# Optimization experiments

Measured on AMD Instinct MI355X. Metric: run time of the kernel, lower is better.

Reference implementation:

```python
import jax, jax.numpy as jnp
import numpy as np

NUM_EMBEDDINGS = 512
EMBEDDING_DIM = 64
COMMITMENT_COST = 0.25


def setup_inputs() -> dict:
    key = jax.random.key(0)
    k1, k2 = jax.random.split(key)
    inputs = jax.random.normal(k1, (256, 2048, EMBEDDING_DIM), dtype=jnp.float32)
    # Glorot uniform for (num_embeddings, embedding_dim)
    limit = np.sqrt(6.0 / (NUM_EMBEDDINGS + EMBEDDING_DIM)).astype(np.float32)
    embeddings = jax.random.uniform(k2, (NUM_EMBEDDINGS, EMBEDDING_DIM),
                                    dtype=jnp.float32, minval=-limit, maxval=limit)
    return {"inputs": inputs, "embeddings": embeddings}


def reference(inputs, embeddings):
    D = embeddings.shape[1]
    flat = inputs.reshape(-1, D)  # [N, D]
    # squared L2 distances via the expanded form (matches the TF code exactly)
    distances = (jnp.sum(flat * flat, axis=1, keepdims=True)
                 + jnp.sum(embeddings * embeddings, axis=1)
                 - 2.0 * flat @ embeddings.T)  # [N, K]
    encoding_indices = jnp.argmin(distances, axis=1)  # [N]
    # direct gather (same math as one-hot matmul, avoids the dense [N,K] matmul)
    quantized = embeddings[encoding_indices].reshape(inputs.shape)
    commitment_loss = COMMITMENT_COST * jnp.mean(
        (jax.lax.stop_gradient(quantized) - inputs) ** 2)
    embedding_loss = jnp.mean((jax.lax.stop_gradient(inputs) - quantized) ** 2)
    # straight-through estimator
    quantized_st = inputs + jax.lax.stop_gradient(quantized - inputs)
    return quantized_st, commitment_loss, embedding_loss
```

## Files before the change

### kernel.cpp

```cpp
#include <hip/hip_runtime.h>
#include <cfloat>

typedef _Float16 f16;
typedef f16 f16x8 __attribute__((ext_vector_type(8)));
typedef float f32x4 __attribute__((ext_vector_type(4)));

#define NTOK (256 * 2048)
#define DDIM 64
#define K 512
#define TPB 256
#define GRID_MAIN 4096
#define GRID_RES  2048
#define THR 1.0e-3f

#define WS_NEEDED 681984

__global__ void vq_pack_kernel(const float* __restrict__ emb, f16* __restrict__ pack) {
    const int chunk = blockIdx.x;
    const int l = threadIdx.x;
    const int split = chunk & 1;
    const int ds = (chunk >> 1) & 1;
    const int ct = chunk >> 2;
    const int code = ct * 16 + (l & 15);
    const int dbase = ds * 32 + (l >> 4) * 8;
    const float* src = emb + (size_t)code * DDIM + dbase;
    f16x8 v;
#pragma unroll
    for (int j = 0; j < 8; ++j) {
        float t = -2.0f * src[j];
        f16 h = (f16)t;
        if (split == 0) v[j] = h;
        else            v[j] = (f16)((t - (float)h) * 2048.0f);
    }
    *(f16x8*)(pack + (size_t)chunk * 512 + (size_t)l * 8) = v;
}

__global__ void vq_senorm_kernel(const float* __restrict__ emb,
                                 float* __restrict__ se) {
    int k = threadIdx.x;
    const float4* e4 = (const float4*)(emb + (size_t)k * DDIM);
    float t[DDIM];
#pragma unroll
    for (int q = 0; q < DDIM / 4; ++q) {
        float4 v = e4[q];
        t[4 * q + 0] = __fmul_rn(v.x, v.x);
        t[4 * q + 1] = __fmul_rn(v.y, v.y);
        t[4 * q + 2] = __fmul_rn(v.z, v.z);
        t[4 * q + 3] = __fmul_rn(v.w, v.w);
    }
#pragma unroll
    for (int s = 1; s < DDIM; s <<= 1)
#pragma unroll
        for (int j = 0; j < DDIM; j += 2 * s) t[j] = __fadd_rn(t[j], t[j + s]);
    se[k] = t[0];
}

#define STAGE_SUPER(buf, s)                                                              \
    do {                                                                                 \
        const char* _g = (const char*)pack + (size_t)(s) * 8192 + (size_t)w * 1024 +     \
                         (size_t)l * 16;                                                 \
        char* _d = (char*)(&Bbuf[(buf)][0]) + (size_t)w * 1024 + (size_t)l * 16;         \
        __builtin_amdgcn_global_load_lds(                                                \
            (const __attribute__((address_space(1))) unsigned int*)_g,                   \
            (__attribute__((address_space(3))) unsigned int*)_d, 16, 0, 0);              \
        __builtin_amdgcn_global_load_lds(                                                \
            (const __attribute__((address_space(1))) unsigned int*)(_g + 4096),          \
            (__attribute__((address_space(3))) unsigned int*)(_d + 4096), 16, 0, 0);     \
    } while (0)

__global__ __launch_bounds__(TPB, 4) void vq_main_kernel(
        const float* __restrict__ xg, const float* __restrict__ emb,
        const f16* __restrict__ pack, const float* __restrict__ se,
        float* __restrict__ out, float* __restrict__ bsum,
        unsigned char* __restrict__ flags) {
    __shared__ f16x8 Bbuf[2][512];
    __shared__ int   kw_lds[4][2][16];
    __shared__ float dw_lds[4][2][16];
    __shared__ float wave_part[4];

    const int tid = threadIdx.x;
    const int w  = tid >> 6;
    const int l  = tid & 63;
    const int lg = l >> 4;
    const int lc = l & 15;
    const size_t base = ((size_t)blockIdx.x * 4 + w) * 32;

    f16x8 Ah[2][2], Al[2][2];
    float sx[2];
#pragma unroll
    for (int i = 0; i < 2; ++i) {
        const float* xp = xg + (base + i * 16 + lc) * DDIM + lg * 8;
        float acc = 0.f;
#pragma unroll
        for (int ds = 0; ds < 2; ++ds) {
            float4 u0 = *(const float4*)(xp + ds * 32);
            float4 u1 = *(const float4*)(xp + ds * 32 + 4);
            float v[8] = {u0.x, u0.y, u0.z, u0.w, u1.x, u1.y, u1.z, u1.w};
            f16x8 h, lo;
#pragma unroll
            for (int j = 0; j < 8; ++j) {
                f16 hh = (f16)v[j];
                h[j]  = hh;
                lo[j] = (f16)((v[j] - (float)hh) * 2048.0f);
                acc = __fmaf_rn(v[j], v[j], acc);
            }
            Ah[i][ds] = h; Al[i][ds] = lo;
        }
        sx[i] = acc;
    }
#pragma unroll
    for (int i = 0; i < 2; ++i) {
        sx[i] += __shfl_xor(sx[i], 16, 64);
        sx[i] += __shfl_xor(sx[i], 32, 64);
    }

    float dmin[2][4], dsec[2][4];
    int   kmin[2][4];
#pragma unroll
    for (int i = 0; i < 2; ++i)
#pragma unroll
        for (int r = 0; r < 4; ++r) { dmin[i][r] = FLT_MAX; dsec[i][r] = FLT_MAX; kmin[i][r] = 0; }

    const int rot = blockIdx.x & 15;
    const float* sebase = se + lc;
    float cs0 = sebase[rot * 32], cs1 = sebase[rot * 32 + 16];
    STAGE_SUPER(0, rot);

    for (int sp = 0; sp < 16; ++sp) {
        const int cur = sp & 1;
        const int s  = (sp + rot) & 15;

        asm volatile("s_waitcnt vmcnt(0)" ::: "memory");
        __builtin_amdgcn_s_barrier();

        float ns0 = 0.f, ns1 = 0.f;
        if (sp < 15) {
            STAGE_SUPER(cur ^ 1, (sp + 1 + rot) & 15);
            const int sn = ((sp + 1 + rot) & 15) * 32;
            ns0 = sebase[sn]; ns1 = sebase[sn + 16];
        }

#pragma unroll
        for (int cl = 0; cl < 2; ++cl) {
            const int ct = s * 2 + cl;
            const int code = ct * 16 + lc;
            const float sek = cl ? cs1 : cs0;
            f16x8 Bh0 = Bbuf[cur][cl * 256 +   0 + l];
            f16x8 Bl0 = Bbuf[cur][cl * 256 +  64 + l];
            f16x8 Bh1 = Bbuf[cur][cl * 256 + 128 + l];
            f16x8 Bl1 = Bbuf[cur][cl * 256 + 192 + l];
#pragma unroll
            for (int i = 0; i < 2; ++i) {
                f32x4 am = {sek, sek, sek, sek};
                f32x4 ac = {0.f, 0.f, 0.f, 0.f};
                am = __builtin_amdgcn_mfma_f32_16x16x32_f16(Ah[i][0], Bh0, am, 0, 0, 0);
                am = __builtin_amdgcn_mfma_f32_16x16x32_f16(Ah[i][1], Bh1, am, 0, 0, 0);
                ac = __builtin_amdgcn_mfma_f32_16x16x32_f16(Al[i][0], Bh0, ac, 0, 0, 0);
                ac = __builtin_amdgcn_mfma_f32_16x16x32_f16(Al[i][1], Bh1, ac, 0, 0, 0);
                ac = __builtin_amdgcn_mfma_f32_16x16x32_f16(Ah[i][0], Bl0, ac, 0, 0, 0);
                ac = __builtin_amdgcn_mfma_f32_16x16x32_f16(Ah[i][1], Bl1, ac, 0, 0, 0);
#pragma unroll
                for (int r = 0; r < 4; ++r) {
                    float v = __fmaf_rn(ac[r], 4.8828125e-4f, am[r]);
                    bool lt = v < dmin[i][r];
                    dsec[i][r] = __builtin_amdgcn_fmed3f(v, dmin[i][r], dsec[i][r]);
                    dmin[i][r] = fminf(v, dmin[i][r]);
                    kmin[i][r] = lt ? code : kmin[i][r];
                }
            }
        }
        cs0 = ns0; cs1 = ns1;
    }

#pragma unroll
    for (int i = 0; i < 2; ++i)
#pragma unroll
        for (int r = 0; r < 4; ++r) {
#pragma unroll
            for (int off = 1; off <= 8; off <<= 1) {
                float dvm = __shfl_xor(dmin[i][r], off, 64);
                int   kvm = __shfl_xor(kmin[i][r], off, 64);
                float dvs = __shfl_xor(dsec[i][r], off, 64);
                bool take = dvm < dmin[i][r];
                float lose = take ? dmin[i][r] : dvm;
                if (take) { dmin[i][r] = dvm; kmin[i][r] = kvm; }
                dsec[i][r] = fminf(fminf(dsec[i][r], dvs), lose);
            }
        }

    if (lc == 0) {
#pragma unroll
        for (int i = 0; i < 2; ++i)
#pragma unroll
            for (int r = 0; r < 4; ++r) {
                int fl = (dsec[i][r] <= dmin[i][r] + THR) ? 1 : 0;
                kw_lds[w][i][lg * 4 + r] = kmin[i][r] | (fl << 31);
                dw_lds[w][i][lg * 4 + r] = dmin[i][r];
                flags[base + i * 16 + lg * 4 + r] = (unsigned char)fl;
            }
    }
    __syncthreads();

#pragma unroll
    for (int m = 0; m < 8; ++m) {
        const int row = m * 4 + (l >> 4);
        const int kwv = kw_lds[w][row >> 4][row & 15] & 0x7fffffff;
        f32x4 vsrc = ((const f32x4*)(emb + (size_t)kwv * DDIM))[lc];
        __builtin_nontemporal_store(vsrc, (f32x4*)(out + (base + row) * DDIM) + lc);
    }

    float lp = 0.f;
    if (l < 16) {
        int k0 = kw_lds[w][0][l], k1 = kw_lds[w][1][l];
        float t0 = (k0 < 0) ? 0.f : __fadd_rn(sx[0], dw_lds[w][0][l]);
        float t1 = (k1 < 0) ? 0.f : __fadd_rn(sx[1], dw_lds[w][1][l]);
        lp = __fadd_rn(t0, t1);
    }
#pragma unroll
    for (int off = 32; off >= 1; off >>= 1) lp += __shfl_down(lp, off, 64);
    if (l == 0) wave_part[w] = lp;
    __syncthreads();
    if (tid == 0) {
        bsum[blockIdx.x] = __fadd_rn(__fadd_rn(wave_part[0], wave_part[1]),
                                     __fadd_rn(wave_part[2], wave_part[3]));
    }
}

__global__ __launch_bounds__(TPB) void vq_rescore_kernel(
        const float* __restrict__ xg, const float* __restrict__ emb,
        const float* __restrict__ se, const unsigned char* __restrict__ flags,
        float* __restrict__ out, float* __restrict__ bsum2) {
    __shared__ int   list[TPB];
    __shared__ float lp_tok[TPB];
    __shared__ int   wcnt[4];
    __shared__ float x_lds[4][DDIM];
    __shared__ float red[TPB / 64];

    const int tid = threadIdx.x;
    const int w = tid >> 6, lane = tid & 63;
    const size_t tok0 = (size_t)blockIdx.x * TPB;
    const int flag = flags[tok0 + tid] != 0;

    lp_tok[tid] = 0.f;
    unsigned long long bal = __ballot(flag);
    if (lane == 0) wcnt[w] = __popcll(bal);
    __syncthreads();
    int off = 0;
#pragma unroll
    for (int ww = 0; ww < 4; ++ww) off += (ww < w) ? wcnt[ww] : 0;
    const int cnt = wcnt[0] + wcnt[1] + wcnt[2] + wcnt[3];
    if (flag) list[off + __popcll(bal & ((1ULL << lane) - 1))] = tid;
    __syncthreads();

    for (int i = w; i < cnt; i += 4) {
        const int tloc = __builtin_amdgcn_readfirstlane(list[i]);
        const size_t tok = tok0 + tloc;

        if (lane < 16)
            ((float4*)&x_lds[w][0])[lane] = ((const float4*)(xg + tok * DDIM))[lane];
        asm volatile("s_waitcnt vmcnt(0) lgkmcnt(0)" ::: "memory");

        float sx;
        {
            float t[DDIM];
#pragma unroll
            for (int j = 0; j < DDIM; ++j) t[j] = __fmul_rn(x_lds[w][j], x_lds[w][j]);
#pragma unroll
            for (int s = 1; s < DDIM; s <<= 1)
#pragma unroll
                for (int j = 0; j < DDIM; j += 2 * s) t[j] = __fadd_rn(t[j], t[j + s]);
            sx = t[0];
        }

        float dmin = FLT_MAX;
        int   kmin = K;
#pragma unroll
        for (int c = 0; c < 8; ++c) {
            const int k = c * 64 + lane;
            const float* ek = emb + (size_t)k * DDIM;
            const float sek = se[k];
            float a0 = 0.f, a1 = 0.f, a2 = 0.f, a3 = 0.f;
#pragma unroll
            for (int j = 0; j < DDIM; j += 4) {
                float4 e4 = *(const float4*)(ek + j);
                a0 = __fmaf_rn(x_lds[w][j + 0], e4.x, a0);
                a1 = __fmaf_rn(x_lds[w][j + 1], e4.y, a1);
                a2 = __fmaf_rn(x_lds[w][j + 2], e4.z, a2);
                a3 = __fmaf_rn(x_lds[w][j + 3], e4.w, a3);
            }
            float dot = __fadd_rn(__fadd_rn(a0, a1), __fadd_rn(a2, a3));
            float d = __fsub_rn(__fadd_rn(sx, sek), __fmul_rn(2.0f, dot));
            if (d < dmin) { dmin = d; kmin = k; }
        }
#pragma unroll
        for (int o = 1; o <= 32; o <<= 1) {
            float dv = __shfl_xor(dmin, o, 64);
            int   kv = __shfl_xor(kmin, o, 64);
            if (dv < dmin || (dv == dmin && kv < kmin)) { dmin = dv; kmin = kv; }
        }

        {
            const float4* esrc = (const float4*)(emb + (size_t)kmin * DDIM);
            if (lane < 16)
                ((float4*)(out + tok * DDIM))[lane] = esrc[lane];
            float lp = 0.f;
#pragma unroll
            for (int q = 0; q < DDIM / 4; ++q) {
                float4 v = esrc[q];
                float d0 = __fsub_rn(v.x, x_lds[w][4 * q + 0]); lp = __fmaf_rn(d0, d0, lp);
                float d1 = __fsub_rn(v.y, x_lds[w][4 * q + 1]); lp = __fmaf_rn(d1, d1, lp);
                float d2 = __fsub_rn(v.z, x_lds[w][4 * q + 2]); lp = __fmaf_rn(d2, d2, lp);
                float d3 = __fsub_rn(v.w, x_lds[w][4 * q + 3]); lp = __fmaf_rn(d3, d3, lp);
            }
            if (lane == 0) lp_tok[tloc] = lp;
        }
    }
    __syncthreads();

    float lp = lp_tok[tid];
#pragma unroll
    for (int o = 32; o >= 1; o >>= 1) lp += __shfl_down(lp, o, 64);
    if (lane == 0) red[w] = lp;
    __syncthreads();
    if (tid == 0) {
        bsum2[blockIdx.x] = __fadd_rn(__fadd_rn(red[0], red[1]),
                                      __fadd_rn(red[2], red[3]));
    }
}

__global__ __launch_bounds__(TPB) void vq_main_f32_kernel(
        const float* __restrict__ xg, const float* __restrict__ emb,
        const float* __restrict__ se, float* __restrict__ out,
        float* __restrict__ bsum) {
    __shared__ int   lds_kmin[TPB];
    __shared__ float lds_red[TPB / 64];
    const int tid = threadIdx.x;
    const size_t tok = (size_t)blockIdx.x * TPB + tid;
    float x[DDIM];
    {
        const float4* xg4 = (const float4*)(xg + tok * DDIM);
#pragma unroll
        for (int q = 0; q < DDIM / 4; ++q) {
            float4 v = xg4[q];
            x[4 * q + 0] = v.x; x[4 * q + 1] = v.y;
            x[4 * q + 2] = v.z; x[4 * q + 3] = v.w;
        }
    }
    float sx;
    {
        float t[DDIM];
#pragma unroll
        for (int j = 0; j < DDIM; ++j) t[j] = __fmul_rn(x[j], x[j]);
#pragma unroll
        for (int s = 1; s < DDIM; s <<= 1)
#pragma unroll
            for (int j = 0; j < DDIM; j += 2 * s) t[j] = __fadd_rn(t[j], t[j + s]);
        sx = t[0];
    }
    float dmin = FLT_MAX; int kmin = 0;
    for (int k = 0; k < K; ++k) {
        const float* ek = emb + (size_t)k * DDIM;
        const float sek = se[k];
        float a0 = 0.f, a1 = 0.f, a2 = 0.f, a3 = 0.f;
#pragma unroll
        for (int j = 0; j < DDIM; j += 4) {
            a0 = __fmaf_rn(x[j + 0], ek[j + 0], a0);
            a1 = __fmaf_rn(x[j + 1], ek[j + 1], a1);
            a2 = __fmaf_rn(x[j + 2], ek[j + 2], a2);
            a3 = __fmaf_rn(x[j + 3], ek[j + 3], a3);
        }
        float dot = __fadd_rn(__fadd_rn(a0, a1), __fadd_rn(a2, a3));
        float d = __fsub_rn(__fadd_rn(sx, sek), __fmul_rn(2.0f, dot));
        if (d < dmin) { dmin = d; kmin = k; }
    }
    float lp = 0.f;
    {
        const float4* e4 = (const float4*)(emb + (size_t)kmin * DDIM);
#pragma unroll
        for (int q = 0; q < DDIM / 4; ++q) {
            float4 v = e4[q];
            float d0 = __fsub_rn(v.x, x[4 * q + 0]); lp = __fmaf_rn(d0, d0, lp);
            float d1 = __fsub_rn(v.y, x[4 * q + 1]); lp = __fmaf_rn(d1, d1, lp);
            float d2 = __fsub_rn(v.z, x[4 * q + 2]); lp = __fmaf_rn(d2, d2, lp);
            float d3 = __fsub_rn(v.w, x[4 * q + 3]); lp = __fmaf_rn(d3, d3, lp);
        }
    }
    lds_kmin[tid] = kmin;
#pragma unroll
    for (int off = 32; off >= 1; off >>= 1) lp += __shfl_down(lp, off, 64);
    if ((tid & 63) == 0) lds_red[tid >> 6] = lp;
    __syncthreads();
    if (tid == 0) {
        float s = lds_red[0];
#pragma unroll
        for (int w = 1; w < TPB / 64; ++w) s = __fadd_rn(s, lds_red[w]);
        bsum[blockIdx.x] = s;
    }
    {
        const float4* emb4 = (const float4*)emb;
        float4* out4 = (float4*)out + (size_t)blockIdx.x * (TPB * DDIM / 4);
#pragma unroll
        for (int it = 0; it < (TPB * DDIM / 4) / TPB; ++it) {
            int m = it * TPB + tid;
            int t = m >> 4, q = m & 15;
            out4[m] = emb4[(size_t)lds_kmin[t] * 16 + q];
        }
    }
}

__global__ void vq_loss_kernel(const float* __restrict__ bsum, int nb1,
                               const float* __restrict__ bsum2, int nb2,
                               float* __restrict__ out_losses) {
    __shared__ float red[256];
    int tid = threadIdx.x;
    float s = 0.f;
    for (int i = tid; i < nb1; i += 256) s = __fadd_rn(s, bsum[i]);
    for (int i = tid; i < nb2; i += 256) s = __fadd_rn(s, bsum2[i]);
    red[tid] = s;
    __syncthreads();
    for (int off = 128; off >= 1; off >>= 1) {
        if (tid < off) red[tid] = __fadd_rn(red[tid], red[tid + off]);
        __syncthreads();
    }
    if (tid == 0) {
        float mean = red[0] / (float)((long long)NTOK * DDIM);
        out_losses[0] = 0.25f * mean;
        out_losses[1] = mean;
    }
}

extern "C" void kernel_launch(void* const* d_in, const int* in_sizes, int n_in,
                              void* d_out, int out_size, void* d_ws, size_t ws_size,
                              hipStream_t stream) {
    const float* xg  = (const float*)d_in[0];
    const float* emb = (const float*)d_in[1];
    float* out = (float*)d_out;
    char* ws = (char*)d_ws;

    if (ws_size >= (size_t)WS_NEEDED) {
        f16*   pack  = (f16*)ws;
        float* se    = (float*)(ws + 131072);
        float* bsum  = (float*)(ws + 133120);
        float* bsum2 = (float*)(ws + 149504);
        unsigned char* flags = (unsigned char*)(ws + 157696);

        vq_pack_kernel<<<128, 64, 0, stream>>>(emb, pack);
        vq_senorm_kernel<<<1, K, 0, stream>>>(emb, se);
        vq_main_kernel<<<GRID_MAIN, TPB, 0, stream>>>(xg, emb, pack, se, out, bsum, flags);
        vq_rescore_kernel<<<GRID_RES, TPB, 0, stream>>>(xg, emb, se, flags, out, bsum2);
        vq_loss_kernel<<<1, 256, 0, stream>>>(bsum, GRID_MAIN, bsum2, GRID_RES,
                                              out + (size_t)NTOK * DDIM);
    } else {
        float* se   = (float*)ws;
        float* bsum = se + K;
        vq_senorm_kernel<<<1, K, 0, stream>>>(emb, se);
        vq_main_f32_kernel<<<NTOK / TPB, TPB, 0, stream>>>(xg, emb, se, out, bsum);
        vq_loss_kernel<<<1, 256, 0, stream>>>(bsum, NTOK / TPB, bsum, 0,
                                              out + (size_t)NTOK * DDIM);
    }
}
```

Measured before the change: 201.2 us.

## Fuse rescore into main kernel, merge prep kernels, triple-buffer codebook staging

```diff
diff --git a/kernel.cpp b/kernel.cpp
--- a/kernel.cpp
+++ b/kernel.cpp
@@ -10,29 +10,47 @@
 #define K 512
 #define TPB 256
 #define GRID_MAIN 4096
-#define GRID_RES  2048
 #define THR 1.0e-3f
 
-#define WS_NEEDED 681984
-
-__global__ void vq_pack_kernel(const float* __restrict__ emb, f16* __restrict__ pack) {
-    const int chunk = blockIdx.x;
-    const int l = threadIdx.x;
-    const int split = chunk & 1;
-    const int ds = (chunk >> 1) & 1;
-    const int ct = chunk >> 2;
-    const int code = ct * 16 + (l & 15);
-    const int dbase = ds * 32 + (l >> 4) * 8;
-    const float* src = emb + (size_t)code * DDIM + dbase;
-    f16x8 v;
-#pragma unroll
-    for (int j = 0; j < 8; ++j) {
-        float t = -2.0f * src[j];
-        f16 h = (f16)t;
-        if (split == 0) v[j] = h;
-        else            v[j] = (f16)((t - (float)h) * 2048.0f);
-    }
-    *(f16x8*)(pack + (size_t)chunk * 512 + (size_t)l * 8) = v;
+#define WS_NEEDED 149504
+
+__global__ void vq_prep_kernel(const float* __restrict__ emb, f16* __restrict__ pack,
+                               float* __restrict__ se) {
+    const int b = blockIdx.x, l = threadIdx.x;
+    if (b < 128) {
+        const int split = b & 1;
+        const int ds = (b >> 1) & 1;
+        const int ct = b >> 2;
+        const int code = ct * 16 + (l & 15);
+        const int dbase = ds * 32 + (l >> 4) * 8;
+        const float* src = emb + (size_t)code * DDIM + dbase;
+        f16x8 v;
+#pragma unroll
+        for (int j = 0; j < 8; ++j) {
+            float t = -2.0f * src[j];
+            f16 h = (f16)t;
+            if (split == 0) v[j] = h;
+            else            v[j] = (f16)((t - (float)h) * 2048.0f);
+        }
+        *(f16x8*)(pack + (size_t)b * 512 + (size_t)l * 8) = v;
+    } else {
+        const int k = (b - 128) * 64 + l;
+        const float4* e4 = (const float4*)(emb + (size_t)k * DDIM);
+        float t[DDIM];
+#pragma unroll
+        for (int q = 0; q < DDIM / 4; ++q) {
+            float4 v = e4[q];
+            t[4 * q + 0] = __fmul_rn(v.x, v.x);
+            t[4 * q + 1] = __fmul_rn(v.y, v.y);
+            t[4 * q + 2] = __fmul_rn(v.z, v.z);
+            t[4 * q + 3] = __fmul_rn(v.w, v.w);
+        }
+#pragma unroll
+        for (int s = 1; s < DDIM; s <<= 1)
+#pragma unroll
+            for (int j = 0; j < DDIM; j += 2 * s) t[j] = __fadd_rn(t[j], t[j + s]);
+        se[k] = t[0];
+    }
 }
 
 __global__ void vq_senorm_kernel(const float* __restrict__ emb,
@@ -55,7 +73,7 @@
     se[k] = t[0];
 }
 
-#define STAGE_SUPER(buf, s)                                                              \
+#define STAGE3(buf, s)                                                                   \
     do {                                                                                 \
         const char* _g = (const char*)pack + (size_t)(s) * 8192 + (size_t)w * 1024 +     \
                          (size_t)l * 16;                                                 \
@@ -71,12 +89,14 @@
 __global__ __launch_bounds__(TPB, 4) void vq_main_kernel(
         const float* __restrict__ xg, const float* __restrict__ emb,
         const f16* __restrict__ pack, const float* __restrict__ se,
-        float* __restrict__ out, float* __restrict__ bsum,
-        unsigned char* __restrict__ flags) {
-    __shared__ f16x8 Bbuf[2][512];
+        float* __restrict__ out, float* __restrict__ bsum) {
+    __shared__ f16x8 Bbuf[3][512];
+    __shared__ float se_lds[K];
     __shared__ int   kw_lds[4][2][16];
     __shared__ float dw_lds[4][2][16];
-    __shared__ float wave_part[4];
+    __shared__ float lp_tok[128];
+    __shared__ int   list_lds[128];
+    __shared__ int   nflag_lds;
 
     const int tid = threadIdx.x;
     const int w  = tid >> 6;
@@ -85,6 +105,9 @@
     const int lc = l & 15;
     const size_t base = ((size_t)blockIdx.x * 4 + w) * 32;
 
+    se_lds[tid] = se[tid];
+    se_lds[tid + 256] = se[tid + 256];
+
     f16x8 Ah[2][2], Al[2][2];
     float sx[2];
 #pragma unroll
@@ -121,30 +144,28 @@
 #pragma unroll
         for (int r = 0; r < 4; ++r) { dmin[i][r] = FLT_MAX; dsec[i][r] = FLT_MAX; kmin[i][r] = 0; }
 
+    __syncthreads();
+
     const int rot = blockIdx.x & 15;
-    const float* sebase = se + lc;
-    float cs0 = sebase[rot * 32], cs1 = sebase[rot * 32 + 16];
-    STAGE_SUPER(0, rot);
+    STAGE3(0, rot);
+    STAGE3(1, (1 + rot) & 15);
 
     for (int sp = 0; sp < 16; ++sp) {
-        const int cur = sp & 1;
+        const int cur = sp % 3;
         const int s  = (sp + rot) & 15;
 
-        asm volatile("s_waitcnt vmcnt(0)" ::: "memory");
+        if (sp < 15) asm volatile("s_waitcnt vmcnt(2)" ::: "memory");
+        else         asm volatile("s_waitcnt vmcnt(0)" ::: "memory");
         __builtin_amdgcn_s_barrier();
-
-        float ns0 = 0.f, ns1 = 0.f;
-        if (sp < 15) {
-            STAGE_SUPER(cur ^ 1, (sp + 1 + rot) & 15);
-            const int sn = ((sp + 1 + rot) & 15) * 32;
-            ns0 = sebase[sn]; ns1 = sebase[sn + 16];
-        }
+        __builtin_amdgcn_sched_barrier(0);
+
+        if (sp < 14) STAGE3((sp + 2) % 3, (sp + 2 + rot) & 15);
 
 #pragma unroll
         for (int cl = 0; cl < 2; ++cl) {
             const int ct = s * 2 + cl;
             const int code = ct * 16 + lc;
-            const float sek = cl ? cs1 : cs0;
+            const float sek = se_lds[ct * 16 + lc];
             f16x8 Bh0 = Bbuf[cur][cl * 256 +   0 + l];
             f16x8 Bl0 = Bbuf[cur][cl * 256 +  64 + l];
             f16x8 Bh1 = Bbuf[cur][cl * 256 + 128 + l];
@@ -169,7 +190,6 @@
                 }
             }
         }
-        cs0 = ns0; cs1 = ns1;
     }
 
 #pragma unroll
@@ -188,6 +208,7 @@
             }
         }
 
+    if (tid == 0) nflag_lds = 0;
     if (lc == 0) {
 #pragma unroll
         for (int i = 0; i < 2; ++i)
@@ -196,7 +217,6 @@
                 int fl = (dsec[i][r] <= dmin[i][r] + THR) ? 1 : 0;
                 kw_lds[w][i][lg * 4 + r] = kmin[i][r] | (fl << 31);
                 dw_lds[w][i][lg * 4 + r] = dmin[i][r];
-                flags[base + i * 16 + lg * 4 + r] = (unsigned char)fl;
             }
     }
     __syncthreads();
@@ -209,123 +229,93 @@
         __builtin_nontemporal_store(vsrc, (f32x4*)(out + (base + row) * DDIM) + lc);
     }
 
-    float lp = 0.f;
     if (l < 16) {
         int k0 = kw_lds[w][0][l], k1 = kw_lds[w][1][l];
-        float t0 = (k0 < 0) ? 0.f : __fadd_rn(sx[0], dw_lds[w][0][l]);
-        float t1 = (k1 < 0) ? 0.f : __fadd_rn(sx[1], dw_lds[w][1][l]);
-        lp = __fadd_rn(t0, t1);
-    }
-#pragma unroll
-    for (int off = 32; off >= 1; off >>= 1) lp += __shfl_down(lp, off, 64);
-    if (l == 0) wave_part[w] = lp;
-    __syncthreads();
-    if (tid == 0) {
-        bsum[blockIdx.x] = __fadd_rn(__fadd_rn(wave_part[0], wave_part[1]),
-                                     __fadd_rn(wave_part[2], wave_part[3]));
-    }
-}
-
-__global__ __launch_bounds__(TPB) void vq_rescore_kernel(
-        const float* __restrict__ xg, const float* __restrict__ emb,
-        const float* __restrict__ se, const unsigned char* __restrict__ flags,
-        float* __restrict__ out, float* __restrict__ bsum2) {
-    __shared__ int   list[TPB];
-    __shared__ float lp_tok[TPB];
-    __shared__ int   wcnt[4];
-    __shared__ float x_lds[4][DDIM];
-    __shared__ float red[TPB / 64];
-
-    const int tid = threadIdx.x;
-    const int w = tid >> 6, lane = tid & 63;
-    const size_t tok0 = (size_t)blockIdx.x * TPB;
-    const int flag = flags[tok0 + tid] != 0;
-
-    lp_tok[tid] = 0.f;
-    unsigned long long bal = __ballot(flag);
-    if (lane == 0) wcnt[w] = __popcll(bal);
-    __syncthreads();
-    int off = 0;
-#pragma unroll
-    for (int ww = 0; ww < 4; ++ww) off += (ww < w) ? wcnt[ww] : 0;
-    const int cnt = wcnt[0] + wcnt[1] + wcnt[2] + wcnt[3];
-    if (flag) list[off + __popcll(bal & ((1ULL << lane) - 1))] = tid;
-    __syncthreads();
-
-    for (int i = w; i < cnt; i += 4) {
-        const int tloc = __builtin_amdgcn_readfirstlane(list[i]);
-        const size_t tok = tok0 + tloc;
-
-        if (lane < 16)
-            ((float4*)&x_lds[w][0])[lane] = ((const float4*)(xg + tok * DDIM))[lane];
+        lp_tok[w * 32 + l]      = (k0 < 0) ? 0.f : __fadd_rn(sx[0], dw_lds[w][0][l]);
+        lp_tok[w * 32 + 16 + l] = (k1 < 0) ? 0.f : __fadd_rn(sx[1], dw_lds[w][1][l]);
+    }
+    if (tid < 128) {
+        if (kw_lds[tid >> 5][(tid >> 4) & 1][tid & 15] < 0)
+            list_lds[atomicAdd(&nflag_lds, 1)] = tid;
+    }
+    __syncthreads();
+
+    const int nf = nflag_lds;
+    float* xrow = (float*)&Bbuf[0][0] + w * DDIM;
+    for (int ii = w; ii < nf; ii += 4) {
+        const int tloc = list_lds[ii];
+        const size_t tok = (size_t)blockIdx.x * 128 + tloc;
+
+        if (l < 16)
+            ((float4*)xrow)[l] = ((const float4*)(xg + tok * DDIM))[l];
         asm volatile("s_waitcnt vmcnt(0) lgkmcnt(0)" ::: "memory");
 
-        float sx;
+        float sxr;
         {
             float t[DDIM];
 #pragma unroll
-            for (int j = 0; j < DDIM; ++j) t[j] = __fmul_rn(x_lds[w][j], x_lds[w][j]);
+            for (int j = 0; j < DDIM; ++j) t[j] = __fmul_rn(xrow[j], xrow[j]);
 #pragma unroll
             for (int s = 1; s < DDIM; s <<= 1)
 #pragma unroll
                 for (int j = 0; j < DDIM; j += 2 * s) t[j] = __fadd_rn(t[j], t[j + s]);
-            sx = t[0];
-        }
-
-        float dmin = FLT_MAX;
-        int   kmin = K;
+            sxr = t[0];
+        }
+
+        float dmn = FLT_MAX;
+        int   kmn = K;
 #pragma unroll
         for (int c = 0; c < 8; ++c) {
-            const int k = c * 64 + lane;
+            const int k = c * 64 + l;
             const float* ek = emb + (size_t)k * DDIM;
-            const float sek = se[k];
+            const float sek = se_lds[k];
             float a0 = 0.f, a1 = 0.f, a2 = 0.f, a3 = 0.f;
 #pragma unroll
             for (int j = 0; j < DDIM; j += 4) {
                 float4 e4 = *(const float4*)(ek + j);
-                a0 = __fmaf_rn(x_lds[w][j + 0], e4.x, a0);
-                a1 = __fmaf_rn(x_lds[w][j + 1], e4.y, a1);
-                a2 = __fmaf_rn(x_lds[w][j + 2], e4.z, a2);
-                a3 = __fmaf_rn(x_lds[w][j + 3], e4.w, a3);
+                a0 = __fmaf_rn(xrow[j + 0], e4.x, a0);
+                a1 = __fmaf_rn(xrow[j + 1], e4.y, a1);
+                a2 = __fmaf_rn(xrow[j + 2], e4.z, a2);
+                a3 = __fmaf_rn(xrow[j + 3], e4.w, a3);
             }
             float dot = __fadd_rn(__fadd_rn(a0, a1), __fadd_rn(a2, a3));
-            float d = __fsub_rn(__fadd_rn(sx, sek), __fmul_rn(2.0f, dot));
-            if (d < dmin) { dmin = d; kmin = k; }
+            float d = __fsub_rn(__fadd_rn(sxr, sek), __fmul_rn(2.0f, dot));
+            if (d < dmn) { dmn = d; kmn = k; }
         }
 #pragma unroll
         for (int o = 1; o <= 32; o <<= 1) {
-            float dv = __shfl_xor(dmin, o, 64);
-            int   kv = __shfl_xor(kmin, o, 64);
-            if (dv < dmin || (dv == dmin && kv < kmin)) { dmin = dv; kmin = kv; }
+            float dv = __shfl_xor(dmn, o, 64);
+            int   kv = __shfl_xor(kmn, o, 64);
+            if (dv < dmn || (dv == dmn && kv < kmn)) { dmn = dv; kmn = kv; }
         }
 
         {
-            const float4* esrc = (const float4*)(emb + (size_t)kmin * DDIM);
-            if (lane < 16)
-                ((float4*)(out + tok * DDIM))[lane] = esrc[lane];
+            const float4* esrc = (const float4*)(emb + (size_t)kmn * DDIM);
+            if (l < 16)
+                ((float4*)(out + tok * DDIM))[l] = esrc[l];
             float lp = 0.f;
 #pragma unroll
             for (int q = 0; q < DDIM / 4; ++q) {
                 float4 v = esrc[q];
-                float d0 = __fsub_rn(v.x, x_lds[w][4 * q + 0]); lp = __fmaf_rn(d0, d0, lp);
-                float d1 = __fsub_rn(v.y, x_lds[w][4 * q + 1]); lp = __fmaf_rn(d1, d1, lp);
-                float d2 = __fsub_rn(v.z, x_lds[w][4 * q + 2]); lp = __fmaf_rn(d2, d2, lp);
-                float d3 = __fsub_rn(v.w, x_lds[w][4 * q + 3]); lp = __fmaf_rn(d3, d3, lp);
-            }
-            if (lane == 0) lp_tok[tloc] = lp;
-        }
-    }
-    __syncthreads();
-
-    float lp = lp_tok[tid];
-#pragma unroll
-    for (int o = 32; o >= 1; o >>= 1) lp += __shfl_down(lp, o, 64);
-    if (lane == 0) red[w] = lp;
-    __syncthreads();
-    if (tid == 0) {
-        bsum2[blockIdx.x] = __fadd_rn(__fadd_rn(red[0], red[1]),
-                                      __fadd_rn(red[2], red[3]));
-    }
+                float d0 = __fsub_rn(v.x, xrow[4 * q + 0]); lp = __fmaf_rn(d0, d0, lp);
+                float d1 = __fsub_rn(v.y, xrow[4 * q + 1]); lp = __fmaf_rn(d1, d1, lp);
+                float d2 = __fsub_rn(v.z, xrow[4 * q + 2]); lp = __fmaf_rn(d2, d2, lp);
+                float d3 = __fsub_rn(v.w, xrow[4 * q + 3]); lp = __fmaf_rn(d3, d3, lp);
+            }
+            if (l == 0) lp_tok[tloc] = lp;
+        }
+    }
+    __syncthreads();
+
+    if (tid < 128) {
+        float lp = lp_tok[tid];
+#pragma unroll
+        for (int o = 32; o >= 1; o >>= 1) lp += __shfl_down(lp, o, 64);
+        if (l == 0) dw_lds[0][0][w] = lp;
+    }
+    __syncthreads();
+    if (tid == 0)
+        bsum[blockIdx.x] = __fadd_rn(dw_lds[0][0][0], dw_lds[0][0][1]);
 }
 
 __global__ __launch_bounds__(TPB) void vq_main_f32_kernel(
@@ -409,13 +399,11 @@
 }
 
 __global__ void vq_loss_kernel(const float* __restrict__ bsum, int nb1,
-                               const float* __restrict__ bsum2, int nb2,
                                float* __restrict__ out_losses) {
     __shared__ float red[256];
     int tid = threadIdx.x;
     float s = 0.f;
     for (int i = tid; i < nb1; i += 256) s = __fadd_rn(s, bsum[i]);
-    for (int i = tid; i < nb2; i += 256) s = __fadd_rn(s, bsum2[i]);
     red[tid] = s;
     __syncthreads();
     for (int off = 128; off >= 1; off >>= 1) {
@@ -438,24 +426,18 @@
     char* ws = (char*)d_ws;
 
     if (ws_size >= (size_t)WS_NEEDED) {
-        f16*   pack  = (f16*)ws;
-        float* se    = (float*)(ws + 131072);
-        float* bsum  = (float*)(ws + 133120);
-        float* bsum2 = (float*)(ws + 149504);
-        unsigned char* flags = (unsigned char*)(ws + 157696);
-
-        vq_pack_kernel<<<128, 64, 0, stream>>>(emb, pack);
-        vq_senorm_kernel<<<1, K, 0, stream>>>(emb, se);
-        vq_main_kernel<<<GRID_MAIN, TPB, 0, stream>>>(xg, emb, pack, se, out, bsum, flags);
-        vq_rescore_kernel<<<GRID_RES, TPB, 0, stream>>>(xg, emb, se, flags, out, bsum2);
-        vq_loss_kernel<<<1, 256, 0, stream>>>(bsum, GRID_MAIN, bsum2, GRID_RES,
-                                              out + (size_t)NTOK * DDIM);
+        f16*   pack = (f16*)ws;
+        float* se   = (float*)(ws + 131072);
+        float* bsum = (float*)(ws + 133120);
+
+        vq_prep_kernel<<<136, 64, 0, stream>>>(emb, pack, se);
+        vq_main_kernel<<<GRID_MAIN, TPB, 0, stream>>>(xg, emb, pack, se, out, bsum);
+        vq_loss_kernel<<<1, 256, 0, stream>>>(bsum, GRID_MAIN, out + (size_t)NTOK * DDIM);
     } else {
         float* se   = (float*)ws;
         float* bsum = se + K;
         vq_senorm_kernel<<<1, K, 0, stream>>>(emb, se);
         vq_main_f32_kernel<<<NTOK / TPB, TPB, 0, stream>>>(xg, emb, se, out, bsum);
-        vq_loss_kernel<<<1, 256, 0, stream>>>(bsum, NTOK / TPB, bsum, 0,
-                                              out + (size_t)NTOK * DDIM);
-    }
-}
+        vq_loss_kernel<<<1, 256, 0, stream>>>(bsum, NTOK / TPB, out + (size_t)NTOK * DDIM);
+    }
+}
```

Result: faster. 192.8 us (-4.2%).

## Merge pack and norm prep kernels; double codebook super-tile per barrier

Applied to the files above, without the earlier changes.

```diff
diff --git a/kernel.cpp b/kernel.cpp
--- a/kernel.cpp
+++ b/kernel.cpp
@@ -15,57 +15,76 @@
 
 #define WS_NEEDED 681984
 
-__global__ void vq_pack_kernel(const float* __restrict__ emb, f16* __restrict__ pack) {
-    const int chunk = blockIdx.x;
-    const int l = threadIdx.x;
-    const int split = chunk & 1;
-    const int ds = (chunk >> 1) & 1;
-    const int ct = chunk >> 2;
-    const int code = ct * 16 + (l & 15);
-    const int dbase = ds * 32 + (l >> 4) * 8;
-    const float* src = emb + (size_t)code * DDIM + dbase;
-    f16x8 v;
-#pragma unroll
-    for (int j = 0; j < 8; ++j) {
-        float t = -2.0f * src[j];
-        f16 h = (f16)t;
-        if (split == 0) v[j] = h;
-        else            v[j] = (f16)((t - (float)h) * 2048.0f);
-    }
-    *(f16x8*)(pack + (size_t)chunk * 512 + (size_t)l * 8) = v;
+__device__ __forceinline__ float sq_tree64(const float* __restrict__ x) {
+    float g0, g1, g2, g3, g4, g5, g6, g7;
+#define GRP(G, dst)                                                                      \
+    do {                                                                                 \
+        float p0 = __fmul_rn(x[8 * G + 0], x[8 * G + 0]);                                \
+        float p1 = __fmul_rn(x[8 * G + 1], x[8 * G + 1]);                                \
+        float p2 = __fmul_rn(x[8 * G + 2], x[8 * G + 2]);                                \
+        float p3 = __fmul_rn(x[8 * G + 3], x[8 * G + 3]);                                \
+        float p4 = __fmul_rn(x[8 * G + 4], x[8 * G + 4]);                                \
+        float p5 = __fmul_rn(x[8 * G + 5], x[8 * G + 5]);                                \
+        float p6 = __fmul_rn(x[8 * G + 6], x[8 * G + 6]);                                \
+        float p7 = __fmul_rn(x[8 * G + 7], x[8 * G + 7]);                                \
+        dst = __fadd_rn(__fadd_rn(__fadd_rn(p0, p1), __fadd_rn(p2, p3)),                 \
+                        __fadd_rn(__fadd_rn(p4, p5), __fadd_rn(p6, p7)));                \
+    } while (0)
+    GRP(0, g0); GRP(1, g1); GRP(2, g2); GRP(3, g3);
+    GRP(4, g4); GRP(5, g5); GRP(6, g6); GRP(7, g7);
+#undef GRP
+    return __fadd_rn(__fadd_rn(__fadd_rn(g0, g1), __fadd_rn(g2, g3)),
+                     __fadd_rn(__fadd_rn(g4, g5), __fadd_rn(g6, g7)));
+}
+
+__global__ void vq_prep_kernel(const float* __restrict__ emb, f16* __restrict__ pack,
+                               float* __restrict__ se) {
+    const int b = blockIdx.x, l = threadIdx.x;
+    if (b < 128) {
+        const int split = b & 1;
+        const int ds = (b >> 1) & 1;
+        const int ct = b >> 2;
+        const int code = ct * 16 + (l & 15);
+        const int dbase = ds * 32 + (l >> 4) * 8;
+        const float* src = emb + (size_t)code * DDIM + dbase;
+        f16x8 v;
+#pragma unroll
+        for (int j = 0; j < 8; ++j) {
+            float t = -2.0f * src[j];
+            f16 h = (f16)t;
+            if (split == 0) v[j] = h;
+            else            v[j] = (f16)((t - (float)h) * 2048.0f);
+        }
+        *(f16x8*)(pack + (size_t)b * 512 + (size_t)l * 8) = v;
+    } else {
+        const int k = (b - 128) * 64 + l;
+        se[k] = sq_tree64(emb + (size_t)k * DDIM);
+    }
 }
 
 __global__ void vq_senorm_kernel(const float* __restrict__ emb,
                                  float* __restrict__ se) {
     int k = threadIdx.x;
-    const float4* e4 = (const float4*)(emb + (size_t)k * DDIM);
-    float t[DDIM];
-#pragma unroll
-    for (int q = 0; q < DDIM / 4; ++q) {
-        float4 v = e4[q];
-        t[4 * q + 0] = __fmul_rn(v.x, v.x);
-        t[4 * q + 1] = __fmul_rn(v.y, v.y);
-        t[4 * q + 2] = __fmul_rn(v.z, v.z);
-        t[4 * q + 3] = __fmul_rn(v.w, v.w);
-    }
-#pragma unroll
-    for (int s = 1; s < DDIM; s <<= 1)
-#pragma unroll
-        for (int j = 0; j < DDIM; j += 2 * s) t[j] = __fadd_rn(t[j], t[j + s]);
-    se[k] = t[0];
+    se[k] = sq_tree64(emb + (size_t)k * DDIM);
 }
 
 #define STAGE_SUPER(buf, s)                                                              \
     do {                                                                                 \
-        const char* _g = (const char*)pack + (size_t)(s) * 8192 + (size_t)w * 1024 +     \
+        const char* _g = (const char*)pack + (size_t)(s) * 16384 + (size_t)w * 4096 +    \
                          (size_t)l * 16;                                                 \
-        char* _d = (char*)(&Bbuf[(buf)][0]) + (size_t)w * 1024 + (size_t)l * 16;         \
+        char* _d = (char*)(&Bbuf[(buf)][0]) + (size_t)w * 4096 + (size_t)l * 16;         \
         __builtin_amdgcn_global_load_lds(                                                \
             (const __attribute__((address_space(1))) unsigned int*)_g,                   \
             (__attribute__((address_space(3))) unsigned int*)_d, 16, 0, 0);              \
         __builtin_amdgcn_global_load_lds(                                                \
-            (const __attribute__((address_space(1))) unsigned int*)(_g + 4096),          \
-            (__attribute__((address_space(3))) unsigned int*)(_d + 4096), 16, 0, 0);     \
+            (const __attribute__((address_space(1))) unsigned int*)(_g + 1024),          \
+            (__attribute__((address_space(3))) unsigned int*)(_d + 1024), 16, 0, 0);     \
+        __builtin_amdgcn_global_load_lds(                                                \
+            (const __attribute__((address_space(1))) unsigned int*)(_g + 2048),          \
+            (__attribute__((address_space(3))) unsigned int*)(_d + 2048), 16, 0, 0);     \
+        __builtin_amdgcn_global_load_lds(                                                \
+            (const __attribute__((address_space(1))) unsigned int*)(_g + 3072),          \
+            (__attribute__((address_space(3))) unsigned int*)(_d + 3072), 16, 0, 0);     \
     } while (0)
 
 __global__ __launch_bounds__(TPB, 4) void vq_main_kernel(
@@ -73,7 +92,7 @@
         const f16* __restrict__ pack, const float* __restrict__ se,
         float* __restrict__ out, float* __restrict__ bsum,
         unsigned char* __restrict__ flags) {
-    __shared__ f16x8 Bbuf[2][512];
+    __shared__ f16x8 Bbuf[2][1024];
     __shared__ int   kw_lds[4][2][16];
     __shared__ float dw_lds[4][2][16];
     __shared__ float wave_part[4];
@@ -121,30 +140,32 @@
 #pragma unroll
         for (int r = 0; r < 4; ++r) { dmin[i][r] = FLT_MAX; dsec[i][r] = FLT_MAX; kmin[i][r] = 0; }
 
-    const int rot = blockIdx.x & 15;
+    const int rot = blockIdx.x & 7;
     const float* sebase = se + lc;
-    float cs0 = sebase[rot * 32], cs1 = sebase[rot * 32 + 16];
+    float cs0 = sebase[rot * 64], cs1 = sebase[rot * 64 + 16],
+          cs2 = sebase[rot * 64 + 32], cs3 = sebase[rot * 64 + 48];
     STAGE_SUPER(0, rot);
 
-    for (int sp = 0; sp < 16; ++sp) {
+    for (int sp = 0; sp < 8; ++sp) {
         const int cur = sp & 1;
-        const int s  = (sp + rot) & 15;
+        const int s  = (sp + rot) & 7;
 
         asm volatile("s_waitcnt vmcnt(0)" ::: "memory");
         __builtin_amdgcn_s_barrier();
 
-        float ns0 = 0.f, ns1 = 0.f;
-        if (sp < 15) {
-            STAGE_SUPER(cur ^ 1, (sp + 1 + rot) & 15);
-            const int sn = ((sp + 1 + rot) & 15) * 32;
+        float ns0 = 0.f, ns1 = 0.f, ns2 = 0.f, ns3 = 0.f;
+        if (sp < 7) {
+            STAGE_SUPER(cur ^ 1, (sp + 1 + rot) & 7);
+            const int sn = ((sp + 1 + rot) & 7) * 64;
             ns0 = sebase[sn]; ns1 = sebase[sn + 16];
-        }
-
-#pragma unroll
-        for (int cl = 0; cl < 2; ++cl) {
-            const int ct = s * 2 + cl;
+            ns2 = sebase[sn + 32]; ns3 = sebase[sn + 48];
+        }
+
+#pragma unroll
+        for (int cl = 0; cl < 4; ++cl) {
+            const int ct = s * 4 + cl;
             const int code = ct * 16 + lc;
-            const float sek = cl ? cs1 : cs0;
+            const float sek = (cl == 0) ? cs0 : (cl == 1) ? cs1 : (cl == 2) ? cs2 : cs3;
             f16x8 Bh0 = Bbuf[cur][cl * 256 +   0 + l];
             f16x8 Bl0 = Bbuf[cur][cl * 256 +  64 + l];
             f16x8 Bh1 = Bbuf[cur][cl * 256 + 128 + l];
@@ -169,7 +190,7 @@
                 }
             }
         }
-        cs0 = ns0; cs1 = ns1;
+        cs0 = ns0; cs1 = ns1; cs2 = ns2; cs3 = ns3;
     }
 
 #pragma unroll
@@ -260,17 +281,7 @@
             ((float4*)&x_lds[w][0])[lane] = ((const float4*)(xg + tok * DDIM))[lane];
         asm volatile("s_waitcnt vmcnt(0) lgkmcnt(0)" ::: "memory");
 
-        float sx;
-        {
-            float t[DDIM];
-#pragma unroll
-            for (int j = 0; j < DDIM; ++j) t[j] = __fmul_rn(x_lds[w][j], x_lds[w][j]);
-#pragma unroll
-            for (int s = 1; s < DDIM; s <<= 1)
-#pragma unroll
-                for (int j = 0; j < DDIM; j += 2 * s) t[j] = __fadd_rn(t[j], t[j + s]);
-            sx = t[0];
-        }
+        const float sx = sq_tree64(&x_lds[w][0]);
 
         float dmin = FLT_MAX;
         int   kmin = K;
@@ -346,17 +357,7 @@
             x[4 * q + 2] = v.z; x[4 * q + 3] = v.w;
         }
     }
-    float sx;
-    {
-        float t[DDIM];
-#pragma unroll
-        for (int j = 0; j < DDIM; ++j) t[j] = __fmul_rn(x[j], x[j]);
-#pragma unroll
-        for (int s = 1; s < DDIM; s <<= 1)
-#pragma unroll
-            for (int j = 0; j < DDIM; j += 2 * s) t[j] = __fadd_rn(t[j], t[j + s]);
-        sx = t[0];
-    }
+    const float sx = sq_tree64(x);
     float dmin = FLT_MAX; int kmin = 0;
     for (int k = 0; k < K; ++k) {
         const float* ek = emb + (size_t)k * DDIM;
@@ -444,8 +445,7 @@
         float* bsum2 = (float*)(ws + 149504);
         unsigned char* flags = (unsigned char*)(ws + 157696);
 
-        vq_pack_kernel<<<128, 64, 0, stream>>>(emb, pack);
-        vq_senorm_kernel<<<1, K, 0, stream>>>(emb, se);
+        vq_prep_kernel<<<136, 64, 0, stream>>>(emb, pack, se);
         vq_main_kernel<<<GRID_MAIN, TPB, 0, stream>>>(xg, emb, pack, se, out, bsum, flags);
         vq_rescore_kernel<<<GRID_RES, TPB, 0, stream>>>(xg, emb, se, flags, out, bsum2);
         vq_loss_kernel<<<1, 256, 0, stream>>>(bsum, GRID_MAIN, bsum2, GRID_RES,
```

New measurement: 190.8 us. -5.2%, faster.
